# Kernel tuning notes

Measured on AMD Instinct MI355X. Metric: run time of the kernel, lower is better.

Reference implementation:

```python
import jax, jax.numpy as jnp
import numpy as np

NN_SIZE = 10          # k for kNN (includes the point itself as its own nearest neighbor)
COS_EPS = 1e-8        # torch.nn.CosineSimilarity eps


def _pairwise_sqdist(p):
    # p: (B,N,3) -> (B,N,N) squared euclidean distances without (B,N,N,3) intermediate
    x2 = jnp.sum(p * p, axis=-1)                      # (B,N)
    inner = jnp.einsum('bnd,bmd->bnm', p, p)          # (B,N,N)
    return x2[:, :, None] + x2[:, None, :] - 2.0 * inner


def _batch_normals(points):
    # points: (B,N,3) -> PCA normals (B,N,3)
    d = _pairwise_sqdist(points)                      # (B,N,N)
    _, idx = jax.lax.top_k(-d, NN_SIZE)               # (B,N,K) indices of k nearest
    nbrs = jax.vmap(lambda p, i: p[i])(points, idx)   # (B,N,K,3) gathered neighborhoods
    centered = nbrs - jnp.mean(nbrs, axis=2, keepdims=True)
    cov = jnp.einsum('bnki,bnkj->bnij', centered, centered) / NN_SIZE  # (B,N,3,3)
    _, vecs = jnp.linalg.eigh(cov)                    # eigenvalues ascending
    return vecs[..., :, 0]                            # eigvec of smallest eigval = normal


def setup_inputs() -> dict:
    key = jax.random.key(0)
    k1, k2 = jax.random.split(key)
    pred = jax.random.normal(k1, (8, 4096, 3), dtype=jnp.float32)
    gt_normals = jax.random.normal(k2, (8, 4096, 3), dtype=jnp.float32)
    return {"pred": pred, "gt_normals": gt_normals}


def reference(pred, gt_normals):
    pred_normals = _batch_normals(pred)                         # (B,N,3)
    dot = jnp.sum(pred_normals * gt_normals, axis=-1)           # (B,N)
    na = jnp.linalg.norm(pred_normals, axis=-1)
    nb = jnp.linalg.norm(gt_normals, axis=-1)
    cos = dot / (jnp.maximum(na, COS_EPS) * jnp.maximum(nb, COS_EPS))
    return jnp.mean(1.0 - cos)
```

## Files before the change

kernel.cpp:

```cpp
#include <hip/hip_runtime.h>
#include <math.h>


#define NPTS   4096
#define KNN    10
#define NBINS  256
#define XLO    (-5.5f)
#define INVBW  (256.0f / 11.0f)
#define W      1536
#define QPB    32
#define NB     1024
#define LISTCAP 32768

__device__ __forceinline__ unsigned int umed3(unsigned int a, unsigned int b, unsigned int c) {
    unsigned int r;
    asm("v_med3_u32 %0, %1, %2, %3" : "=v"(r) : "v"(a), "v"(b), "v"(c));
    return r;
}

__device__ __forceinline__ void sift(unsigned int nd[KNN], unsigned int key) {
#pragma unroll
    for (int t = KNN - 1; t >= 1; --t)
        nd[t] = umed3(key, nd[t - 1], nd[t]);
    nd[0] = nd[0] < key ? nd[0] : key;
}

__device__ __forceinline__ int xbin(float x) {
    int bin = (int)floorf((x - XLO) * INVBW);
    return bin < 0 ? 0 : (bin > NBINS - 1 ? NBINS - 1 : bin);
}

#define MAKE_KEY(q, c, J)                                                     \
    ({                                                                        \
        float sw_ = (q).w + (c).w;                                            \
        float dp_ = fmaf((q).x, (c).x, fmaf((q).y, (c).y, (q).z * (c).z));    \
        float d_  = fmaf(-2.0f, dp_, sw_);                                    \
        d_ = fmaxf(d_, 0.0f);                                                 \
        (__float_as_uint(d_) & 0xFFFFF000u) | (unsigned)(J);                  \
    })

__device__ float normal_loss3(const float nbx[KNN], const float nby[KNN],
                              const float nbz[KNN], const float* g3)
{
    float sx = 0.f, sy = 0.f, sz = 0.f;
#pragma unroll
    for (int t = 0; t < KNN; ++t) { sx += nbx[t]; sy += nby[t]; sz += nbz[t]; }
    float mx = sx / 10.0f, my = sy / 10.0f, mz = sz / 10.0f;
    float c00 = 0.f, c01 = 0.f, c02 = 0.f, c11 = 0.f, c12 = 0.f, c22 = 0.f;
#pragma unroll
    for (int t = 0; t < KNN; ++t) {
        float ux = nbx[t] - mx, uy = nby[t] - my, uz = nbz[t] - mz;
        c00 = fmaf(ux, ux, c00);
        c01 = fmaf(ux, uy, c01);
        c02 = fmaf(ux, uz, c02);
        c11 = fmaf(uy, uy, c11);
        c12 = fmaf(uy, uz, c12);
        c22 = fmaf(uz, uz, c22);
    }
    double a00 = (double)(c00 / 10.0f), a01 = (double)(c01 / 10.0f);
    double a02 = (double)(c02 / 10.0f), a11 = (double)(c11 / 10.0f);
    double a12 = (double)(c12 / 10.0f), a22 = (double)(c22 / 10.0f);

    double vx = 1.0, vy = 0.0, vz = 0.0;
    double qd = (a00 + a11 + a22) / 3.0;
    double p1 = a01 * a01 + a02 * a02 + a12 * a12;
    double b00 = a00 - qd, b11 = a11 - qd, b22 = a22 - qd;
    double p2 = b00 * b00 + b11 * b11 + b22 * b22 + 2.0 * p1;
    if (p2 > 1e-300) {
        double p = sqrt(p2 / 6.0);
        double inv = 1.0 / p;
        double m00 = b00 * inv, m01 = a01 * inv, m02 = a02 * inv;
        double m11 = b11 * inv, m12 = a12 * inv, m22 = b22 * inv;
        double detB = m00 * (m11 * m22 - m12 * m12)
                    - m01 * (m01 * m22 - m12 * m02)
                    + m02 * (m01 * m12 - m11 * m02);
        double r = 0.5 * detB;
        r = r < -1.0 ? -1.0 : (r > 1.0 ? 1.0 : r);
        double phi = acos(r) / 3.0;
        double eig0 = qd + 2.0 * p * cos(phi + 2.0943951023931953);
        double r0x = a00 - eig0, r0y = a01, r0z = a02;
        double r1y = a11 - eig0, r1z = a12;
        double r2z = a22 - eig0;
        double c0x = r0y * r1z - r0z * r1y;
        double c0y = r0z * r0y - r0x * r1z;
        double c0z = r0x * r1y - r0y * r0y;
        double c1x = r0y * r2z - r0z * r1z;
        double c1y = r0z * r0z - r0x * r2z;
        double c1z = r0x * r1z - r0y * r0z;
        double c2x = r1y * r2z - r1z * r1z;
        double c2y = r1z * r0z - r0y * r2z;
        double c2z = r0y * r1z - r1y * r0z;
        double n0 = c0x * c0x + c0y * c0y + c0z * c0z;
        double n1 = c1x * c1x + c1y * c1y + c1z * c1z;
        double n2 = c2x * c2x + c2y * c2y + c2z * c2z;
        double bx, by, bz, bn;
        if (n0 >= n1 && n0 >= n2) { bx = c0x; by = c0y; bz = c0z; bn = n0; }
        else if (n1 >= n2)        { bx = c1x; by = c1y; bz = c1z; bn = n1; }
        else                      { bx = c2x; by = c2y; bz = c2z; bn = n2; }
        if (bn > 1e-300) {
            double s = 1.0 / sqrt(bn);
            vx = bx * s; vy = by * s; vz = bz * s;
        }
    }
    float nx = (float)vx, ny = (float)vy, nz = (float)vz;
    float gx = g3[0], gy = g3[1], gz = g3[2];
    float dotg = nx * gx + ny * gy + nz * gz;
    float na = sqrtf(nx * nx + ny * ny + nz * nz);
    float gn = sqrtf(gx * gx + gy * gy + gz * gz);
    float cs = dotg / (fmaxf(na, 1e-8f) * fmaxf(gn, 1e-8f));
    return 1.0f - cs;
}

__global__ __launch_bounds__(1024) void gtnl_bin(
    const float* __restrict__ pred, float4* __restrict__ wsPts,
    unsigned int* __restrict__ wsCnt)
{
    __shared__ unsigned int hist[NBINS];
    __shared__ unsigned int bst[NBINS + 1];

    const int tid = threadIdx.x;
    const int b   = blockIdx.x;
    if (b == 0 && tid == 0) wsCnt[0] = 0;
    const float* src = pred + (size_t)b * NPTS * 3;

    if (tid < NBINS) hist[tid] = 0;
    __syncthreads();

    float px[4], py[4], pz[4];
    int   pb[4], pidx[4];
#pragma unroll
    for (int k = 0; k < 4; ++k) {
        int p = tid + 1024 * k;
        float x = src[3 * p + 0];
        float y = src[3 * p + 1];
        float z = src[3 * p + 2];
        int bin = xbin(x);
        px[k] = x; py[k] = y; pz[k] = z; pb[k] = bin; pidx[k] = p;
        atomicAdd(&hist[bin], 1u);
    }
    __syncthreads();

    if (tid < 64) {
        unsigned s0 = hist[4 * tid + 0], s1 = hist[4 * tid + 1];
        unsigned s2 = hist[4 * tid + 2], s3 = hist[4 * tid + 3];
        unsigned tot = s0 + s1 + s2 + s3;
        unsigned pre = tot;
#pragma unroll
        for (int d = 1; d < 64; d <<= 1) {
            unsigned t = __shfl_up(pre, d, 64);
            if (tid >= d) pre += t;
        }
        unsigned ex = pre - tot;
        bst[4 * tid + 0] = ex;
        bst[4 * tid + 1] = ex + s0;
        bst[4 * tid + 2] = ex + s0 + s1;
        bst[4 * tid + 3] = ex + s0 + s1 + s2;
        if (tid == 63) bst[NBINS] = ex + tot;
    }
    __syncthreads();

    if (tid < NBINS) hist[tid] = bst[tid];
    __syncthreads();

#pragma unroll
    for (int k = 0; k < 4; ++k) {
        unsigned pos = atomicAdd(&hist[pb[k]], 1u);
        wsPts[(size_t)b * NPTS + pos] =
            make_float4(px[k], py[k], pz[k], __uint_as_float((unsigned)pidx[k]));
    }
}

__global__ __launch_bounds__(256, 4) void gtnl_scan(
    const float4* __restrict__ wsPts, const float* __restrict__ gt,
    float* __restrict__ qloss, unsigned int* __restrict__ wsCnt,
    unsigned int* __restrict__ wsList)
{
    __shared__ float4 pts[W];
    __shared__ unsigned int mbuf[7][QPB][KNN];

    const int tid   = threadIdx.x;
    const int bid   = blockIdx.x;
    const int b     = bid >> 7;
    const int chunk = bid & 127;
    const int qbase = chunk * QPB;
    const int s     = tid >> 5;
    const int ql    = tid & 31;

    int W0 = qbase + QPB / 2 - W / 2;
    W0 = W0 < 0 ? 0 : (W0 > NPTS - W ? NPTS - W : W0);

    const float4* wp = wsPts + (size_t)b * NPTS;
    for (int i = tid; i < W; i += 256) {
        float4 v = wp[W0 + i];
        pts[i] = make_float4(v.x, v.y, v.z, fmaf(v.x, v.x, fmaf(v.y, v.y, v.z * v.z)));
    }
    __syncthreads();

    const int qpos = qbase + ql;
    const float4 q = pts[qpos - W0];

    unsigned int nd[KNN];
#pragma unroll
    for (int t = 0; t < KNN; ++t) nd[t] = 0x7F000000u;

#pragma unroll 8
    for (int t = 0; t < W / 8; ++t) {
        int j = 8 * t + s;
        float4 c = pts[j];
        sift(nd, MAKE_KEY(q, c, j));
    }

    if (s != 0) {
#pragma unroll
        for (int t = 0; t < KNN; ++t) mbuf[s - 1][ql][t] = nd[t];
    }
    __syncthreads();
    if (s != 0) return;

#pragma unroll
    for (int m = 0; m < 7; ++m)
#pragma unroll
        for (int t = 0; t < KNN; ++t) sift(nd, mbuf[m][ql][t]);

    unsigned int thr_bits = (nd[KNN - 1] & 0xFFFFF000u) + 0x1000u;
    float thr = __uint_as_float(thr_bits);
    float hw  = __uint_as_float(__float_as_uint(sqrtf(thr)) + 4) + 1e-3f;
    bool okL = (W0 == 0)        || (q.x - hw > pts[0].x);
    bool okR = (W0 == NPTS - W) || (q.x + hw < pts[W - 1].x);

    const unsigned int qorig = __float_as_uint(wp[qpos].w);
    float res = 0.0f;
    if (okL && okR) {
        float nbx[KNN], nby[KNN], nbz[KNN];
#pragma unroll
        for (int t = 0; t < KNN; ++t) {
            float4 pn = pts[nd[t] & 0xFFFu];
            nbx[t] = pn.x; nby[t] = pn.y; nbz[t] = pn.z;
        }
        res = normal_loss3(nbx, nby, nbz, gt + ((size_t)b * NPTS + qorig) * 3);
    } else {
        unsigned int idx = atomicAdd(wsCnt, 1u);
        wsList[idx] = ((unsigned)b << 12) | (unsigned)qpos;
    }
    qloss[(size_t)b * NPTS + qorig] = res;
}

__global__ __launch_bounds__(256, 4) void gtnl_fix(
    const float4* __restrict__ wsPts, const float* __restrict__ gt,
    float* __restrict__ qloss, const unsigned int* __restrict__ wsCnt,
    const unsigned int* __restrict__ wsList)
{
    const int lane = threadIdx.x & 63;
    const int wid  = blockIdx.x * 4 + (threadIdx.x >> 6);
    unsigned int n = wsCnt[0];

    for (unsigned int i = wid; i < n; i += 4096) {
        unsigned int e = wsList[i];
        const int b    = e >> 12;
        const int qpos = e & 0xFFF;
        const float4* wp = wsPts + (size_t)b * NPTS;

        float4 qv = wp[qpos];
        float4 q  = make_float4(qv.x, qv.y, qv.z,
                                fmaf(qv.x, qv.x, fmaf(qv.y, qv.y, qv.z * qv.z)));
        const unsigned int qorig = __float_as_uint(qv.w);

        unsigned int nd[KNN];
#pragma unroll
        for (int t = 0; t < KNN; ++t) nd[t] = 0x7F000000u;

#pragma unroll 8
        for (int t = 0; t < NPTS / 64; ++t) {
            int j = 64 * t + lane;
            float4 v = wp[j];
            float4 c = make_float4(v.x, v.y, v.z,
                                   fmaf(v.x, v.x, fmaf(v.y, v.y, v.z * v.z)));
            sift(nd, MAKE_KEY(q, c, j));
        }

        unsigned int keys[KNN];
#pragma unroll
        for (int r = 0; r < KNN; ++r) {
            unsigned int m = nd[0];
#pragma unroll
            for (int d = 1; d < 64; d <<= 1) {
                unsigned int o = __shfl_xor(m, d, 64);
                m = m < o ? m : o;
            }
            keys[r] = m;
            bool win = (nd[0] == m);
#pragma unroll
            for (int t = 0; t < KNN - 1; ++t) nd[t] = win ? nd[t + 1] : nd[t];
            nd[KNN - 1] = win ? 0xFFFFFFFFu : nd[KNN - 1];
        }

        float nbx[KNN], nby[KNN], nbz[KNN];
#pragma unroll
        for (int t = 0; t < KNN; ++t) {
            float4 pn = wp[keys[t] & 0xFFFu];
            nbx[t] = pn.x; nby[t] = pn.y; nbz[t] = pn.z;
        }
        float res = normal_loss3(nbx, nby, nbz, gt + ((size_t)b * NPTS + qorig) * 3);
        if (lane == 0) qloss[(size_t)b * NPTS + qorig] = res;
    }
}

__global__ __launch_bounds__(1024) void gtnl_reduceQ(
    const float* __restrict__ qloss, float* __restrict__ out)
{
    __shared__ float sbuf[1024];
    const int tid = threadIdx.x;
    const float4* q4 = (const float4*)qloss;
    float s = 0.0f;
#pragma unroll
    for (int t = 0; t < 8; ++t) {
        float4 v = q4[tid + 1024 * t];
        s += (v.x + v.y) + (v.z + v.w);
    }
    sbuf[tid] = s;
    __syncthreads();
    for (int k = 512; k > 0; k >>= 1) {
        if (tid < k) sbuf[tid] += sbuf[tid + k];
        __syncthreads();
    }
    if (tid == 0) out[0] = sbuf[0] / 32768.0f;
}

__global__ __launch_bounds__(256) void gtnl_brute(
    const float* __restrict__ pred, const float* __restrict__ gt,
    float* __restrict__ partial)
{
    __shared__ float4 ptsB[NPTS];
    __shared__ unsigned int mbuf[64][3][KNN];

    const int tid = threadIdx.x;
    const int b   = blockIdx.x >> 6;
    const int qc  = blockIdx.x & 63;
    const int ql  = tid & 63;
    const int sub = tid >> 6;
    const int qi  = qc * 64 + ql;

    const float* src = pred + (size_t)b * NPTS * 3;
    for (int p = tid; p < NPTS; p += 256) {
        float x = src[3 * p + 0], y = src[3 * p + 1], z = src[3 * p + 2];
        ptsB[p] = make_float4(x, y, z, fmaf(x, x, fmaf(y, y, z * z)));
    }
    __syncthreads();

    const float4 q = ptsB[qi];
    unsigned int nd[KNN];
#pragma unroll
    for (int t = 0; t < KNN; ++t) nd[t] = 0xFFFFFFFFu;

    const int j0 = sub * 1024;
#pragma unroll 8
    for (int j = j0; j < j0 + 1024; ++j) {
        float4 c = ptsB[j];
        sift(nd, MAKE_KEY(q, c, j));
    }

    if (sub != 0) {
#pragma unroll
        for (int t = 0; t < KNN; ++t) mbuf[ql][sub - 1][t] = nd[t];
    }
    __syncthreads();

    float res = 0.0f;
    if (sub == 0) {
#pragma unroll
        for (int ss = 0; ss < 3; ++ss)
#pragma unroll
            for (int t = 0; t < KNN; ++t) sift(nd, mbuf[ql][ss][t]);
        float nbx[KNN], nby[KNN], nbz[KNN];
#pragma unroll
        for (int t = 0; t < KNN; ++t) {
            float4 pn = ptsB[nd[t] & 0xFFFu];
            nbx[t] = pn.x; nby[t] = pn.y; nbz[t] = pn.z;
        }
        res = normal_loss3(nbx, nby, nbz, gt + ((size_t)b * NPTS + qi) * 3);
#pragma unroll
        for (int d = 32; d > 0; d >>= 1) res += __shfl_xor(res, d, 64);
    }
    __syncthreads();
    if (tid == 0) partial[blockIdx.x] = res;
}

__global__ __launch_bounds__(512) void gtnl_reduceP(
    const float* __restrict__ partial, float* __restrict__ out)
{
    __shared__ float sb[512];
    const int tid = threadIdx.x;
    sb[tid] = partial[tid];
    __syncthreads();
    for (int k = 256; k > 0; k >>= 1) {
        if (tid < k) sb[tid] += sb[tid + k];
        __syncthreads();
    }
    if (tid == 0) out[0] = sb[0] / 32768.0f;
}

extern "C" void kernel_launch(void* const* d_in, const int* in_sizes, int n_in,
                              void* d_out, int out_size, void* d_ws, size_t ws_size,
                              hipStream_t stream) {
    const float* pred = (const float*)d_in[0];
    const float* gt   = (const float*)d_in[1];
    float* out        = (float*)d_out;

    const size_t PTS_BYTES   = (size_t)8 * NPTS * sizeof(float4);
    const size_t QLOSS_BYTES = (size_t)8 * NPTS * sizeof(float);
    const size_t LIST_BYTES  = (size_t)LISTCAP * sizeof(unsigned);
    const size_t NEED = PTS_BYTES + QLOSS_BYTES + LIST_BYTES + 64;

    if (ws_size >= NEED) {
        float4*       wsPts  = (float4*)d_ws;
        float*        qloss  = (float*)((char*)d_ws + PTS_BYTES);
        unsigned int* wsList = (unsigned int*)((char*)d_ws + PTS_BYTES + QLOSS_BYTES);
        unsigned int* wsCnt  = (unsigned int*)((char*)d_ws + PTS_BYTES + QLOSS_BYTES + LIST_BYTES);

        gtnl_bin<<<8, 1024, 0, stream>>>(pred, wsPts, wsCnt);
        gtnl_scan<<<NB, 256, 0, stream>>>(wsPts, gt, qloss, wsCnt, wsList);
        gtnl_fix<<<NB, 256, 0, stream>>>(wsPts, gt, qloss, wsCnt, wsList);
        gtnl_reduceQ<<<1, 1024, 0, stream>>>(qloss, out);
    } else {
        float* partial = (float*)d_ws;
        gtnl_brute<<<512, 256, 0, stream>>>(pred, gt, partial);
        gtnl_reduceP<<<1, 512, 0, stream>>>(partial, out);
    }
}
```

Before: 53.91 us.

## Use fp32 eigen-solve and merge kNN sub-lists with butterfly shuffles

Switches the closed-form 3x3 eigen solve from double to float, with multiply-by-reciprocal and rsqrt in place of divisions. The scan kernel now interleaves 8 sub-scanners per query within a wavefront and merges their top-k lists through xor shuffles instead of an LDS buffer and a barrier. All 8 lanes then compute the loss redundantly and only lane 0 writes it. Occupancy hint raised to 8 blocks and the loop unroll reduced; fp32 eigenvectors risk accuracy loss on near-degenerate covariances.

```diff
diff --git a/kernel.cpp b/kernel.cpp
--- a/kernel.cpp
+++ b/kernel.cpp
@@ -39,13 +39,13 @@
         (__float_as_uint(d_) & 0xFFFFF000u) | (unsigned)(J);                  \
     })
 
-__device__ float normal_loss3(const float nbx[KNN], const float nby[KNN],
-                              const float nbz[KNN], const float* g3)
+__device__ float normal_loss3f(const float nbx[KNN], const float nby[KNN],
+                               const float nbz[KNN], const float* g3)
 {
     float sx = 0.f, sy = 0.f, sz = 0.f;
 #pragma unroll
     for (int t = 0; t < KNN; ++t) { sx += nbx[t]; sy += nby[t]; sz += nbz[t]; }
-    float mx = sx / 10.0f, my = sy / 10.0f, mz = sz / 10.0f;
+    float mx = sx * 0.1f, my = sy * 0.1f, mz = sz * 0.1f;
     float c00 = 0.f, c01 = 0.f, c02 = 0.f, c11 = 0.f, c12 = 0.f, c22 = 0.f;
 #pragma unroll
     for (int t = 0; t < KNN; ++t) {
@@ -57,55 +57,53 @@
         c12 = fmaf(uy, uz, c12);
         c22 = fmaf(uz, uz, c22);
     }
-    double a00 = (double)(c00 / 10.0f), a01 = (double)(c01 / 10.0f);
-    double a02 = (double)(c02 / 10.0f), a11 = (double)(c11 / 10.0f);
-    double a12 = (double)(c12 / 10.0f), a22 = (double)(c22 / 10.0f);
-
-    double vx = 1.0, vy = 0.0, vz = 0.0;
-    double qd = (a00 + a11 + a22) / 3.0;
-    double p1 = a01 * a01 + a02 * a02 + a12 * a12;
-    double b00 = a00 - qd, b11 = a11 - qd, b22 = a22 - qd;
-    double p2 = b00 * b00 + b11 * b11 + b22 * b22 + 2.0 * p1;
-    if (p2 > 1e-300) {
-        double p = sqrt(p2 / 6.0);
-        double inv = 1.0 / p;
-        double m00 = b00 * inv, m01 = a01 * inv, m02 = a02 * inv;
-        double m11 = b11 * inv, m12 = a12 * inv, m22 = b22 * inv;
-        double detB = m00 * (m11 * m22 - m12 * m12)
-                    - m01 * (m01 * m22 - m12 * m02)
-                    + m02 * (m01 * m12 - m11 * m02);
-        double r = 0.5 * detB;
-        r = r < -1.0 ? -1.0 : (r > 1.0 ? 1.0 : r);
-        double phi = acos(r) / 3.0;
-        double eig0 = qd + 2.0 * p * cos(phi + 2.0943951023931953);
-        double r0x = a00 - eig0, r0y = a01, r0z = a02;
-        double r1y = a11 - eig0, r1z = a12;
-        double r2z = a22 - eig0;
-        double c0x = r0y * r1z - r0z * r1y;
-        double c0y = r0z * r0y - r0x * r1z;
-        double c0z = r0x * r1y - r0y * r0y;
-        double c1x = r0y * r2z - r0z * r1z;
-        double c1y = r0z * r0z - r0x * r2z;
-        double c1z = r0x * r1z - r0y * r0z;
-        double c2x = r1y * r2z - r1z * r1z;
-        double c2y = r1z * r0z - r0y * r2z;
-        double c2z = r0y * r1z - r1y * r0z;
-        double n0 = c0x * c0x + c0y * c0y + c0z * c0z;
-        double n1 = c1x * c1x + c1y * c1y + c1z * c1z;
-        double n2 = c2x * c2x + c2y * c2y + c2z * c2z;
-        double bx, by, bz, bn;
+    float a00 = c00 * 0.1f, a01 = c01 * 0.1f, a02 = c02 * 0.1f;
+    float a11 = c11 * 0.1f, a12 = c12 * 0.1f, a22 = c22 * 0.1f;
+
+    float vx = 1.0f, vy = 0.0f, vz = 0.0f;
+    float qd = (a00 + a11 + a22) * (1.0f / 3.0f);
+    float p1 = a01 * a01 + a02 * a02 + a12 * a12;
+    float b00 = a00 - qd, b11 = a11 - qd, b22 = a22 - qd;
+    float p2 = b00 * b00 + b11 * b11 + b22 * b22 + 2.0f * p1;
+    if (p2 > 1e-30f) {
+        float p   = sqrtf(p2 * (1.0f / 6.0f));
+        float inv = 1.0f / p;
+        float m00 = b00 * inv, m01 = a01 * inv, m02 = a02 * inv;
+        float m11 = b11 * inv, m12 = a12 * inv, m22 = b22 * inv;
+        float detB = m00 * (m11 * m22 - m12 * m12)
+                   - m01 * (m01 * m22 - m12 * m02)
+                   + m02 * (m01 * m12 - m11 * m02);
+        float r = 0.5f * detB;
+        r = r < -1.0f ? -1.0f : (r > 1.0f ? 1.0f : r);
+        float phi  = acosf(r) * (1.0f / 3.0f);
+        float eig0 = qd + 2.0f * p * cosf(phi + 2.0943951023931953f);
+        float r0x = a00 - eig0, r0y = a01, r0z = a02;
+        float r1y = a11 - eig0, r1z = a12;
+        float r2z = a22 - eig0;
+        float c0x = r0y * r1z - r0z * r1y;
+        float c0y = r0z * r0y - r0x * r1z;
+        float c0z = r0x * r1y - r0y * r0y;
+        float c1x = r0y * r2z - r0z * r1z;
+        float c1y = r0z * r0z - r0x * r2z;
+        float c1z = r0x * r1z - r0y * r0z;
+        float c2x = r1y * r2z - r1z * r1z;
+        float c2y = r1z * r0z - r0y * r2z;
+        float c2z = r0y * r1z - r1y * r0z;
+        float n0 = c0x * c0x + c0y * c0y + c0z * c0z;
+        float n1 = c1x * c1x + c1y * c1y + c1z * c1z;
+        float n2 = c2x * c2x + c2y * c2y + c2z * c2z;
+        float bx, by, bz, bn;
         if (n0 >= n1 && n0 >= n2) { bx = c0x; by = c0y; bz = c0z; bn = n0; }
         else if (n1 >= n2)        { bx = c1x; by = c1y; bz = c1z; bn = n1; }
         else                      { bx = c2x; by = c2y; bz = c2z; bn = n2; }
-        if (bn > 1e-300) {
-            double s = 1.0 / sqrt(bn);
+        if (bn > 1e-30f) {
+            float s = rsqrtf(bn);
             vx = bx * s; vy = by * s; vz = bz * s;
         }
     }
-    float nx = (float)vx, ny = (float)vy, nz = (float)vz;
     float gx = g3[0], gy = g3[1], gz = g3[2];
-    float dotg = nx * gx + ny * gy + nz * gz;
-    float na = sqrtf(nx * nx + ny * ny + nz * nz);
+    float dotg = vx * gx + vy * gy + vz * gz;
+    float na = sqrtf(vx * vx + vy * vy + vz * vz);
     float gn = sqrtf(gx * gx + gy * gy + gz * gz);
     float cs = dotg / (fmaxf(na, 1e-8f) * fmaxf(gn, 1e-8f));
     return 1.0f - cs;
@@ -170,21 +168,20 @@
     }
 }
 
-__global__ __launch_bounds__(256, 4) void gtnl_scan(
+__global__ __launch_bounds__(256, 8) void gtnl_scan(
     const float4* __restrict__ wsPts, const float* __restrict__ gt,
     float* __restrict__ qloss, unsigned int* __restrict__ wsCnt,
     unsigned int* __restrict__ wsList)
 {
     __shared__ float4 pts[W];
-    __shared__ unsigned int mbuf[7][QPB][KNN];
 
     const int tid   = threadIdx.x;
     const int bid   = blockIdx.x;
     const int b     = bid >> 7;
     const int chunk = bid & 127;
     const int qbase = chunk * QPB;
-    const int s     = tid >> 5;
-    const int ql    = tid & 31;
+    const int s     = tid & 7;
+    const int ql    = tid >> 3;
 
     int W0 = qbase + QPB / 2 - W / 2;
     W0 = W0 < 0 ? 0 : (W0 > NPTS - W ? NPTS - W : W0);
@@ -203,24 +200,24 @@
 #pragma unroll
     for (int t = 0; t < KNN; ++t) nd[t] = 0x7F000000u;
 
-#pragma unroll 8
+#pragma unroll 2
     for (int t = 0; t < W / 8; ++t) {
         int j = 8 * t + s;
         float4 c = pts[j];
         sift(nd, MAKE_KEY(q, c, j));
     }
 
-    if (s != 0) {
-#pragma unroll
-        for (int t = 0; t < KNN; ++t) mbuf[s - 1][ql][t] = nd[t];
-    }
-    __syncthreads();
-    if (s != 0) return;
-
-#pragma unroll
-    for (int m = 0; m < 7; ++m)
-#pragma unroll
-        for (int t = 0; t < KNN; ++t) sift(nd, mbuf[m][ql][t]);
+#pragma unroll
+    for (int r = 1; r <= 4; r <<= 1) {
+        unsigned int tmp[KNN];
+#pragma unroll
+        for (int t = 0; t < KNN; ++t) tmp[t] = nd[t];
+#pragma unroll
+        for (int t = 0; t < KNN; ++t) {
+            unsigned int pk = (unsigned int)__shfl_xor((int)tmp[t], r, 64);
+            sift(nd, pk);
+        }
+    }
 
     unsigned int thr_bits = (nd[KNN - 1] & 0xFFFFF000u) + 0x1000u;
     float thr = __uint_as_float(thr_bits);
@@ -229,7 +226,6 @@
     bool okR = (W0 == NPTS - W) || (q.x + hw < pts[W - 1].x);
 
     const unsigned int qorig = __float_as_uint(wp[qpos].w);
-    float res = 0.0f;
     if (okL && okR) {
         float nbx[KNN], nby[KNN], nbz[KNN];
 #pragma unroll
@@ -237,12 +233,15 @@
             float4 pn = pts[nd[t] & 0xFFFu];
             nbx[t] = pn.x; nby[t] = pn.y; nbz[t] = pn.z;
         }
-        res = normal_loss3(nbx, nby, nbz, gt + ((size_t)b * NPTS + qorig) * 3);
+        float res = normal_loss3f(nbx, nby, nbz, gt + ((size_t)b * NPTS + qorig) * 3);
+        if (s == 0) qloss[(size_t)b * NPTS + qorig] = res;
     } else {
-        unsigned int idx = atomicAdd(wsCnt, 1u);
-        wsList[idx] = ((unsigned)b << 12) | (unsigned)qpos;
-    }
-    qloss[(size_t)b * NPTS + qorig] = res;
+        if (s == 0) {
+            unsigned int idx = atomicAdd(wsCnt, 1u);
+            wsList[idx] = ((unsigned)b << 12) | (unsigned)qpos;
+            qloss[(size_t)b * NPTS + qorig] = 0.0f;
+        }
+    }
 }
 
 __global__ __launch_bounds__(256, 4) void gtnl_fix(
@@ -300,7 +299,7 @@
             float4 pn = wp[keys[t] & 0xFFFu];
             nbx[t] = pn.x; nby[t] = pn.y; nbz[t] = pn.z;
         }
-        float res = normal_loss3(nbx, nby, nbz, gt + ((size_t)b * NPTS + qorig) * 3);
+        float res = normal_loss3f(nbx, nby, nbz, gt + ((size_t)b * NPTS + qorig) * 3);
         if (lane == 0) qloss[(size_t)b * NPTS + qorig] = res;
     }
 }
@@ -377,7 +376,7 @@
             float4 pn = ptsB[nd[t] & 0xFFFu];
             nbx[t] = pn.x; nby[t] = pn.y; nbz[t] = pn.z;
         }
-        res = normal_loss3(nbx, nby, nbz, gt + ((size_t)b * NPTS + qi) * 3);
+        res = normal_loss3f(nbx, nby, nbz, gt + ((size_t)b * NPTS + qi) * 3);
 #pragma unroll
         for (int d = 32; d > 0; d >>= 1) res += __shfl_xor(res, d, 64);
     }
```

Measured after the change: 54.19 us. Within noise of the previous version (+0.5%).
